# Performance work log

Measured on AMD Instinct MI355X. Metric: run time of the kernel, lower is better.

## Reference

```python
import jax, jax.numpy as jnp
import numpy as np

STATE_LEN = 256
EPS = 1e-5


def _ln(x, g, b):
    m = jnp.mean(x, axis=-1, keepdims=True)
    v = jnp.mean((x - m) ** 2, axis=-1, keepdims=True)
    return (x - m) / jnp.sqrt(v + EPS) * g + b


def setup_inputs() -> dict:
    key = jax.random.key(0)
    ks = jax.random.split(key, 12)
    B, S, L, D, DK, DV = 2, 256, 2048, 512, 64, 64
    T = L + 2 * S  # 2560
    def w(k, i, o):
        return jax.random.normal(k, (i, o), jnp.float32) * 0.02
    return {
        "x": jax.random.normal(ks[0], (B, T, D), jnp.float32),
        "w_q": w(ks[1], D, DK), "w_k": w(ks[2], D, DK), "w_v": w(ks[3], D, DV),
        "w_q_ss": w(ks[4], D, DK), "w_k_ss": w(ks[5], D, DK), "w_v_ss": w(ks[6], D, DV),
        "w_q_se": w(ks[7], D, DK), "w_k_se": w(ks[8], D, DK), "w_v_se": w(ks[9], D, DV),
        "ln_g": jnp.ones((D,), jnp.float32), "ln_b": jnp.zeros((D,), jnp.float32),
        "ln_g_ss": jnp.ones((D,), jnp.float32), "ln_b_ss": jnp.zeros((D,), jnp.float32),
        "ln_g_se": jnp.ones((D,), jnp.float32), "ln_b_se": jnp.zeros((D,), jnp.float32),
        "cope_emb": jax.random.normal(ks[10], (1, DK, T), jnp.float32),
    }


def reference(x, w_q, w_k, w_v, w_q_ss, w_k_ss, w_v_ss, w_q_se, w_k_se, w_v_se,
              ln_g, ln_b, ln_g_ss, ln_b_ss, ln_g_se, ln_b_se, cope_emb):
    S = STATE_LEN
    T = x.shape[1]
    # extract_state: [state_start | main | state_end]
    xs, xm, xe = x[:, :S], x[:, S:T - S], x[:, T - S:]
    xm = _ln(xm, ln_g, ln_b)
    xs = _ln(xs, ln_g_ss, ln_b_ss)
    xe = _ln(xe, ln_g_se, ln_b_se)
    q = jnp.concatenate([xs @ w_q_ss, xm @ w_q, xe @ w_q_se], axis=1)  # [B,T,DK]
    k = jnp.concatenate([xs @ w_k_ss, xm @ w_k, xe @ w_k_se], axis=1)
    v = jnp.concatenate([xs @ w_v_ss, xm @ w_v, xe @ w_v_se], axis=1)
    dk = q.shape[-1]
    # --- CoPE bias ---
    logits = jnp.einsum('btd,bsd->bts', q, k)  # [B,T,T]
    gates = jax.nn.sigmoid(logits)
    # reverse cumsum along keys (flip-cumsum-flip)
    pos = jnp.flip(jnp.cumsum(jnp.flip(gates, -1), axis=-1), -1)
    pos = jnp.minimum(pos, jnp.float32(T - 1))
    pf = jnp.floor(pos)
    pc = jnp.ceil(pos)
    li = jnp.einsum('btd,dm->btm', q, cope_emb[0])  # [B,T,T]
    lc = jnp.take_along_axis(li, pc.astype(jnp.int32), axis=-1)
    lf = jnp.take_along_axis(li, pf.astype(jnp.int32), axis=-1)
    w = pos - pf
    bias = lc * w + lf * (1.0 - w)
    # --- attention with tril-log mask + CoPE bias ---
    causal = jnp.tril(jnp.ones((T, T), dtype=bool))
    att_logits = logits / jnp.sqrt(jnp.float32(dk)) + jnp.where(causal, bias, -jnp.inf)
    attn = jax.nn.softmax(att_logits, axis=-1)
    return jnp.einsum('bts,bsd->btd', attn, v)
```

## Files before the change

### kernel.cpp

```cpp
#include <hip/hip_runtime.h>
#include <hip/hip_bf16.h>
#include <math.h>

using short8 = __attribute__((ext_vector_type(8))) short;
using f32x4  = __attribute__((ext_vector_type(4))) float;

constexpr int S_LEN  = 256;
constexpr int T      = 2560;
constexpr int D_IN   = 512;
constexpr int DK     = 64;
constexpr int B_N    = 2;
constexpr int SS     = 16;

__global__ __launch_bounds__(256) void lnprep_kernel(
    const float* __restrict__ x,
    const float* __restrict__ g_m,  const float* __restrict__ b_m,
    const float* __restrict__ g_s,  const float* __restrict__ b_s,
    const float* __restrict__ g_e,  const float* __restrict__ b_e,
    const float* __restrict__ w_qs, const float* __restrict__ w_ks, const float* __restrict__ w_vs,
    const float* __restrict__ w_q,  const float* __restrict__ w_k,  const float* __restrict__ w_v,
    const float* __restrict__ w_qe, const float* __restrict__ w_ke, const float* __restrict__ w_ve,
    const float* __restrict__ cope,
    __hip_bfloat16* __restrict__ xnh, __hip_bfloat16* __restrict__ xnl,
    __hip_bfloat16* __restrict__ wth, __hip_bfloat16* __restrict__ wtl,
    __hip_bfloat16* __restrict__ copeT)
{
    constexpr int LN_BLOCKS = (B_N * T) / 4;
    if (blockIdx.x < LN_BLOCKS) {
        const int wv   = threadIdx.x >> 6;
        const int lane = threadIdx.x & 63;
        const int row  = blockIdx.x * 4 + wv;
        const int t    = row % T;

        const float *gv, *bv;
        if (t < S_LEN)          { gv = g_s; bv = b_s; }
        else if (t < T - S_LEN) { gv = g_m; bv = b_m; }
        else                    { gv = g_e; bv = b_e; }

        const float4* xr4 = (const float4*)(x + (size_t)row * D_IN);
        float4 a = xr4[lane * 2], b4 = xr4[lane * 2 + 1];
        float xv[8] = {a.x, a.y, a.z, a.w, b4.x, b4.y, b4.z, b4.w};

        float s = 0.f;
#pragma unroll
        for (int j = 0; j < 8; ++j) s += xv[j];
#pragma unroll
        for (int off = 32; off > 0; off >>= 1) s += __shfl_down(s, off);
        s = __shfl(s, 0);
        const float mean = s * (1.0f / D_IN);

        float sq = 0.f;
#pragma unroll
        for (int j = 0; j < 8; ++j) { float d = xv[j] - mean; sq += d * d; }
#pragma unroll
        for (int off = 32; off > 0; off >>= 1) sq += __shfl_down(sq, off);
        sq = __shfl(sq, 0);
        const float inv = rsqrtf(sq * (1.0f / D_IN) + 1e-5f);

        const float4* gv4 = (const float4*)gv;
        const float4* bv4 = (const float4*)bv;
        float4 ga = gv4[lane * 2], gb = gv4[lane * 2 + 1];
        float4 ba = bv4[lane * 2], bb = bv4[lane * 2 + 1];
        float g8[8] = {ga.x, ga.y, ga.z, ga.w, gb.x, gb.y, gb.z, gb.w};
        float b8[8] = {ba.x, ba.y, ba.z, ba.w, bb.x, bb.y, bb.z, bb.w};

        short hs[8], ls[8];
#pragma unroll
        for (int j = 0; j < 8; ++j) {
            float v = (xv[j] - mean) * inv * g8[j] + b8[j];
            __hip_bfloat16 h  = __float2bfloat16(v);
            __hip_bfloat16 lo = __float2bfloat16(v - __bfloat162float(h));
            hs[j] = *(short*)&h;
            ls[j] = *(short*)&lo;
        }
        short8 H = {hs[0],hs[1],hs[2],hs[3],hs[4],hs[5],hs[6],hs[7]};
        short8 L = {ls[0],ls[1],ls[2],ls[3],ls[4],ls[5],ls[6],ls[7]};
        *(short8*)(xnh + (size_t)row * D_IN + lane * 8) = H;
        *(short8*)(xnl + (size_t)row * D_IN + lane * 8) = L;
        return;
    }

    const int i = (blockIdx.x - LN_BLOCKS) * 256 + threadIdx.x;
    constexpr int NW = 9 * DK * D_IN;
    if (i < NW) {
        const int matIdx = i >> 15;
        const int rem = i & 32767;
        const int col = rem >> 9, k = rem & 511;
        const float* W =
            (matIdx == 0) ? w_qs : (matIdx == 1) ? w_ks : (matIdx == 2) ? w_vs :
            (matIdx == 3) ? w_q  : (matIdx == 4) ? w_k  : (matIdx == 5) ? w_v  :
            (matIdx == 6) ? w_qe : (matIdx == 7) ? w_ke : w_ve;
        float f = W[(size_t)k * DK + col];
        __hip_bfloat16 h = __float2bfloat16(f);
        wth[i] = h;
        wtl[i] = __float2bfloat16(f - __bfloat162float(h));
    } else if (i < NW + T * DK) {
        const int j = i - NW;
        const int m = j >> 6, d = j & 63;
        copeT[j] = __float2bfloat16(cope[(size_t)d * T + m]);
    }
}

__global__ __launch_bounds__(256) void qkv_gemm_kernel(
    const __hip_bfloat16* __restrict__ xnh, const __hip_bfloat16* __restrict__ xnl,
    const __hip_bfloat16* __restrict__ wth, const __hip_bfloat16* __restrict__ wtl,
    __hip_bfloat16* __restrict__ qh, __hip_bfloat16* __restrict__ ql,
    __hip_bfloat16* __restrict__ kh, __hip_bfloat16* __restrict__ kl,
    __hip_bfloat16* __restrict__ vT)
{
    const int bid = blockIdx.x;
    const int mt = bid / 3, mat = bid % 3;
    const int r0 = mt * 64;
    const int b  = r0 / T, t0 = r0 % T;
    const int region = (t0 < S_LEN) ? 0 : (t0 < T - S_LEN) ? 1 : 2;
    const int matIdx = region * 3 + mat;

    const int tid = threadIdx.x, lane = tid & 63, wid = tid >> 6;
    const int wm = wid >> 1, wn = wid & 1;
    const int fr = lane & 15, k8 = (lane >> 4) * 8;

    f32x4 acc[2][2];
#pragma unroll
    for (int mf = 0; mf < 2; ++mf)
#pragma unroll
        for (int nf = 0; nf < 2; ++nf) acc[mf][nf] = (f32x4){0.f, 0.f, 0.f, 0.f};

    for (int ks = 0; ks < D_IN / 32; ++ks) {
        const int k = ks * 32 + k8;
        short8 ah[2], al[2], bh2[2], bl2[2];
#pragma unroll
        for (int mf = 0; mf < 2; ++mf) {
            size_t off = (size_t)(r0 + wm * 32 + mf * 16 + fr) * D_IN + k;
            ah[mf] = *(const short8*)(xnh + off);
            al[mf] = *(const short8*)(xnl + off);
        }
#pragma unroll
        for (int nf = 0; nf < 2; ++nf) {
            size_t off = ((size_t)matIdx * DK + wn * 32 + nf * 16 + fr) * D_IN + k;
            bh2[nf] = *(const short8*)(wth + off);
            bl2[nf] = *(const short8*)(wtl + off);
        }
#pragma unroll
        for (int mf = 0; mf < 2; ++mf)
#pragma unroll
            for (int nf = 0; nf < 2; ++nf) {
                acc[mf][nf] = __builtin_amdgcn_mfma_f32_16x16x32_bf16(ah[mf], bh2[nf], acc[mf][nf], 0, 0, 0);
                acc[mf][nf] = __builtin_amdgcn_mfma_f32_16x16x32_bf16(ah[mf], bl2[nf], acc[mf][nf], 0, 0, 0);
                acc[mf][nf] = __builtin_amdgcn_mfma_f32_16x16x32_bf16(al[mf], bh2[nf], acc[mf][nf], 0, 0, 0);
            }
    }

    const int r4 = (lane >> 4) * 4;
#pragma unroll
    for (int mf = 0; mf < 2; ++mf)
#pragma unroll
        for (int nf = 0; nf < 2; ++nf) {
            const int cg = wn * 32 + nf * 16 + fr;
#pragma unroll
            for (int j = 0; j < 4; ++j) {
                const int rg = r0 + wm * 32 + mf * 16 + r4 + j;
                float f = acc[mf][nf][j];
                __hip_bfloat16 h  = __float2bfloat16(f);
                __hip_bfloat16 lo = __float2bfloat16(f - __bfloat162float(h));
                if (mat == 0)      { qh[(size_t)rg * DK + cg] = h; ql[(size_t)rg * DK + cg] = lo; }
                else if (mat == 1) { kh[(size_t)rg * DK + cg] = h; kl[(size_t)rg * DK + cg] = lo; }
                else               { vT[((size_t)b * DK + cg) * T + (rg % T)] = h; }
            }
        }
}

__global__ __launch_bounds__(256) void gemm1_kernel(
    const __hip_bfloat16* __restrict__ qh, const __hip_bfloat16* __restrict__ ql,
    const __hip_bfloat16* __restrict__ kh, const __hip_bfloat16* __restrict__ kl,
    const __hip_bfloat16* __restrict__ copeT,
    float* __restrict__ logc, __hip_bfloat16* __restrict__ lic,
    int b0, int t_off, int TC)
{
    constexpr int TS = T / 64;
    const int per_b = (TC / 128) * TS;
    const int bb  = blockIdx.x / per_b;
    const int rem = blockIdx.x % per_b;
    const int ti  = rem / TS, si = rem % TS;
    const int t0  = ti * 128, s0 = si * 64;
    const int b   = b0 + bb;
    float*          logits_c = logc + (size_t)bb * TC * T;
    __hip_bfloat16* li_c     = lic  + (size_t)bb * TC * T;

    const int tid = threadIdx.x, lane = tid & 63, wid = tid >> 6;
    const int wm  = wid >> 1, wn = wid & 1;
    const int fr  = lane & 15, k8 = (lane >> 4) * 8;
    const size_t qb = (size_t)b * T * DK;

    short8 ah[4][2], al[4][2];
#pragma unroll
    for (int mf = 0; mf < 4; ++mf)
#pragma unroll
        for (int ks = 0; ks < 2; ++ks) {
            size_t off = qb + (size_t)(t_off + t0 + wm * 64 + mf * 16 + fr) * DK + ks * 32 + k8;
            ah[mf][ks] = *(const short8*)(qh + off);
            al[mf][ks] = *(const short8*)(ql + off);
        }
    short8 bh[2][2], bl[2][2], bc[2][2];
#pragma unroll
    for (int nf = 0; nf < 2; ++nf)
#pragma unroll
        for (int ks = 0; ks < 2; ++ks) {
            size_t off = (size_t)(s0 + wn * 32 + nf * 16 + fr) * DK + ks * 32 + k8;
            bh[nf][ks] = *(const short8*)(kh + qb + off);
            bl[nf][ks] = *(const short8*)(kl + qb + off);
            bc[nf][ks] = *(const short8*)(copeT + off);
        }

    f32x4 accL[4][2], accM[4][2];
#pragma unroll
    for (int mf = 0; mf < 4; ++mf)
#pragma unroll
        for (int nf = 0; nf < 2; ++nf) {
            accL[mf][nf] = (f32x4){0.f, 0.f, 0.f, 0.f};
            accM[mf][nf] = (f32x4){0.f, 0.f, 0.f, 0.f};
        }

#pragma unroll
    for (int mf = 0; mf < 4; ++mf)
#pragma unroll
        for (int nf = 0; nf < 2; ++nf)
#pragma unroll
            for (int ks = 0; ks < 2; ++ks) {
                accL[mf][nf] = __builtin_amdgcn_mfma_f32_16x16x32_bf16(ah[mf][ks], bh[nf][ks], accL[mf][nf], 0, 0, 0);
                accL[mf][nf] = __builtin_amdgcn_mfma_f32_16x16x32_bf16(ah[mf][ks], bl[nf][ks], accL[mf][nf], 0, 0, 0);
                accL[mf][nf] = __builtin_amdgcn_mfma_f32_16x16x32_bf16(al[mf][ks], bh[nf][ks], accL[mf][nf], 0, 0, 0);
                accM[mf][nf] = __builtin_amdgcn_mfma_f32_16x16x32_bf16(ah[mf][ks], bc[nf][ks], accM[mf][nf], 0, 0, 0);
            }

    const int r4 = (lane >> 4) * 4;
#pragma unroll
    for (int mf = 0; mf < 4; ++mf)
#pragma unroll
        for (int nf = 0; nf < 2; ++nf) {
            const int cg = s0 + wn * 32 + nf * 16 + fr;
#pragma unroll
            for (int j = 0; j < 4; ++j) {
                const int rl = t0 + wm * 64 + mf * 16 + r4 + j;
                const size_t o = (size_t)rl * T + cg;
                logits_c[o] = accL[mf][nf][j];
                li_c[o]     = __float2bfloat16(accM[mf][nf][j]);
            }
        }
}

__global__ __launch_bounds__(256) void phase2_kernel(
    const float* __restrict__ logc, __hip_bfloat16* __restrict__ lic,
    int t_off, int TC)
{
    constexpr int CH = T / 256;
    const int tid  = threadIdx.x;
    const int lane = tid & 63;
    const int wv   = tid >> 6;
    const int bb   = blockIdx.x / TC;
    const int rl   = blockIdx.x % TC;
    const int t    = t_off + rl;

    __shared__ __hip_bfloat16 sli[T];
    __shared__ float redS[4], redM[4], redE[4];

    const float*    lrow  = logc + ((size_t)bb * TC + rl) * T;
    __hip_bfloat16* lirow = lic  + ((size_t)bb * TC + rl) * T;

#pragma unroll
    for (int i = 0; i < 5; ++i) {
        const int idx = i * 256 + tid;
        ((unsigned int*)sli)[idx] = ((const unsigned int*)lirow)[idx];
    }

    const int s0 = tid * CH;
    float lg[CH], g[CH];
    float lsum = 0.f;
    const float2* lr2 = (const float2*)(lrow + s0);
#pragma unroll
    for (int i = 0; i < 5; ++i) {
        float2 v = lr2[i];
        lg[2 * i] = v.x; lg[2 * i + 1] = v.y;
    }
#pragma unroll
    for (int i = 0; i < CH; ++i) {
        g[i] = 1.0f / (1.0f + __expf(-lg[i]));
        lsum += g[i];
    }

    float incl = lsum;
#pragma unroll
    for (int off = 1; off < 64; off <<= 1) {
        float n = __shfl_up(incl, off);
        if (lane >= off) incl += n;
    }
    if (lane == 63) redS[wv] = incl;
    __syncthreads();
    float total = 0.f, wpre = 0.f;
#pragma unroll
    for (int w2 = 0; w2 < 4; ++w2) {
        float tw = redS[w2];
        total += tw;
        if (w2 < wv) wpre += tw;
    }
    float run = wpre + incl - lsum;

    float att[CH];
    float lmax = -INFINITY;
#pragma unroll
    for (int i = 0; i < CH; ++i) {
        int s = s0 + i;
        float pos = total - run;
        run += g[i];
        pos = fminf(pos, (float)(T - 1));
        float pf = floorf(pos);
        float w  = pos - pf;
        int ipf  = (int)pf;
        int ipc  = (int)ceilf(pos);
        float bias = __bfloat162float(sli[ipc]) * w
                   + __bfloat162float(sli[ipf]) * (1.0f - w);
        float al = lg[i] * 0.125f + bias;
        if (s > t) al = -INFINITY;
        att[i] = al;
        lmax = fmaxf(lmax, al);
    }

#pragma unroll
    for (int off = 32; off > 0; off >>= 1) lmax = fmaxf(lmax, __shfl_down(lmax, off));
    if (lane == 0) redM[wv] = lmax;
    __syncthreads();
    const float bmax = fmaxf(fmaxf(redM[0], redM[1]), fmaxf(redM[2], redM[3]));

    float e[CH];
    float esum = 0.f;
#pragma unroll
    for (int i = 0; i < CH; ++i) {
        e[i] = __expf(att[i] - bmax);
        esum += e[i];
    }
#pragma unroll
    for (int off = 32; off > 0; off >>= 1) esum += __shfl_down(esum, off);
    if (lane == 0) redE[wv] = esum;
    __syncthreads();
    const float rden = 1.0f / (redE[0] + redE[1] + redE[2] + redE[3]);

    unsigned int pw[5];
#pragma unroll
    for (int i = 0; i < 5; ++i) {
        __hip_bfloat16 p0 = __float2bfloat16(e[2 * i] * rden);
        __hip_bfloat16 p1 = __float2bfloat16(e[2 * i + 1] * rden);
        pw[i] = (unsigned int)*(unsigned short*)&p0
              | ((unsigned int)*(unsigned short*)&p1 << 16);
    }
    unsigned int* dst = (unsigned int*)(lirow + s0);
#pragma unroll
    for (int i = 0; i < 5; ++i) dst[i] = pw[i];
}

__global__ __launch_bounds__(256) void gemm2_kernel(
    const __hip_bfloat16* __restrict__ lic, const __hip_bfloat16* __restrict__ vT,
    float* __restrict__ out, int b0, int t_off, int TC)
{
    const int per_b = (TC / 128) * SS;
    const int bb  = blockIdx.x / per_b;
    const int rem = blockIdx.x % per_b;
    const int ti  = rem / SS, sc = rem % SS;
    const int t0  = ti * 128;
    const int sb  = sc * (T / SS);
    if (sb > t_off + t0 + 127) return;
    const int b   = b0 + bb;
    const __hip_bfloat16* p_c = lic + (size_t)bb * TC * T;

    const int tid = threadIdx.x, lane = tid & 63, wid = tid >> 6;
    const int wm  = wid >> 1, wn = wid & 1;
    const int fr  = lane & 15, k8 = (lane >> 4) * 8;
    const size_t vb = (size_t)b * DK * T;

    f32x4 acc[4][2];
#pragma unroll
    for (int mf = 0; mf < 4; ++mf)
#pragma unroll
        for (int nf = 0; nf < 2; ++nf) acc[mf][nf] = (f32x4){0.f, 0.f, 0.f, 0.f};

    for (int ks = 0; ks < (T / SS) / 32; ++ks) {
        const int s = sb + ks * 32 + k8;
        short8 a_p[4], bv[2];
#pragma unroll
        for (int mf = 0; mf < 4; ++mf)
            a_p[mf] = *(const short8*)(p_c + (size_t)(t0 + wm * 64 + mf * 16 + fr) * T + s);
#pragma unroll
        for (int nf = 0; nf < 2; ++nf)
            bv[nf] = *(const short8*)(vT + vb + (size_t)(wn * 32 + nf * 16 + fr) * T + s);
#pragma unroll
        for (int mf = 0; mf < 4; ++mf)
#pragma unroll
            for (int nf = 0; nf < 2; ++nf)
                acc[mf][nf] = __builtin_amdgcn_mfma_f32_16x16x32_bf16(a_p[mf], bv[nf], acc[mf][nf], 0, 0, 0);
    }

    const int r4 = (lane >> 4) * 4;
#pragma unroll
    for (int mf = 0; mf < 4; ++mf)
#pragma unroll
        for (int nf = 0; nf < 2; ++nf) {
            const int cg = wn * 32 + nf * 16 + fr;
#pragma unroll
            for (int j = 0; j < 4; ++j) {
                const int rl = t0 + wm * 64 + mf * 16 + r4 + j;
                atomicAdd(&out[((size_t)b * T + t_off + rl) * DK + cg], acc[mf][nf][j]);
            }
        }
}

extern "C" void kernel_launch(void* const* d_in, const int* in_sizes, int n_in,
                              void* d_out, int out_size, void* d_ws, size_t ws_size,
                              hipStream_t stream)
{
    const float* x    = (const float*)d_in[0];
    const float* w_q  = (const float*)d_in[1];
    const float* w_k  = (const float*)d_in[2];
    const float* w_v  = (const float*)d_in[3];
    const float* w_qs = (const float*)d_in[4];
    const float* w_ks = (const float*)d_in[5];
    const float* w_vs = (const float*)d_in[6];
    const float* w_qe = (const float*)d_in[7];
    const float* w_ke = (const float*)d_in[8];
    const float* w_ve = (const float*)d_in[9];
    const float* g_m  = (const float*)d_in[10];
    const float* b_m  = (const float*)d_in[11];
    const float* g_s  = (const float*)d_in[12];
    const float* b_s  = (const float*)d_in[13];
    const float* g_e  = (const float*)d_in[14];
    const float* b_e  = (const float*)d_in[15];
    const float* cope = (const float*)d_in[16];

    const size_t n_qk  = (size_t)B_N * T * DK;
    const size_t n_xn  = (size_t)B_N * T * D_IN;
    const size_t n_wt  = (size_t)9 * DK * D_IN;
    const size_t fixedB = 5 * n_qk * 2 + (size_t)T * DK * 2
                        + 2 * n_xn * 2 + 2 * n_wt * 2;
    auto chunkB = [&](size_t TC) -> size_t {
        return TC * (size_t)T * 4
             + TC * (size_t)T * 2;
    };
    int TC, NB;
    if (fixedB + 2 * chunkB(T) <= ws_size)       { TC = T;    NB = 2; }
    else if (fixedB + chunkB(T) <= ws_size)      { TC = T;    NB = 1; }
    else if (fixedB + chunkB(1280) <= ws_size)   { TC = 1280; NB = 1; }
    else                                         { TC = 640;  NB = 1; }

    char* w = (char*)d_ws;
    __hip_bfloat16* qh    = (__hip_bfloat16*)w; w += n_qk * 2;
    __hip_bfloat16* ql    = (__hip_bfloat16*)w; w += n_qk * 2;
    __hip_bfloat16* kh    = (__hip_bfloat16*)w; w += n_qk * 2;
    __hip_bfloat16* kl    = (__hip_bfloat16*)w; w += n_qk * 2;
    __hip_bfloat16* vT    = (__hip_bfloat16*)w; w += n_qk * 2;
    __hip_bfloat16* copeT = (__hip_bfloat16*)w; w += (size_t)T * DK * 2;
    __hip_bfloat16* xnh   = (__hip_bfloat16*)w; w += n_xn * 2;
    __hip_bfloat16* xnl   = (__hip_bfloat16*)w; w += n_xn * 2;
    __hip_bfloat16* wth   = (__hip_bfloat16*)w; w += n_wt * 2;
    __hip_bfloat16* wtl   = (__hip_bfloat16*)w; w += n_wt * 2;
    float*          logc  = (float*)w;          w += (size_t)NB * TC * T * 4;
    __hip_bfloat16* lic   = (__hip_bfloat16*)w; w += (size_t)NB * TC * T * 2;

    hipMemsetAsync(d_out, 0, (size_t)out_size * sizeof(float), stream);

    constexpr int LN_BLOCKS   = (B_N * T) / 4;
    const int     PREP_BLOCKS = (int)((n_wt + (size_t)T * DK + 255) / 256);
    lnprep_kernel<<<LN_BLOCKS + PREP_BLOCKS, 256, 0, stream>>>(
        x, g_m, b_m, g_s, b_s, g_e, b_e,
        w_qs, w_ks, w_vs, w_q, w_k, w_v, w_qe, w_ke, w_ve, cope,
        xnh, xnl, wth, wtl, copeT);

    qkv_gemm_kernel<<<(B_N * T / 64) * 3, 256, 0, stream>>>(
        xnh, xnl, wth, wtl, qh, ql, kh, kl, vT);

    for (int b0 = 0; b0 < B_N; b0 += NB)
        for (int t_off = 0; t_off < T; t_off += TC) {
            gemm1_kernel<<<NB * (TC / 128) * (T / 64), 256, 0, stream>>>(
                qh, ql, kh, kl, copeT, logc, lic, b0, t_off, TC);
            phase2_kernel<<<NB * TC, 256, 0, stream>>>(
                logc, lic, t_off, TC);
            gemm2_kernel<<<NB * (TC / 128) * SS, 256, 0, stream>>>(
                lic, vT, (float*)d_out, b0, t_off, TC);
        }
}
```

Measured before the change: 107.2 us.

## Fuse attention stages into one cooperative persistent kernel and fold output zeroing into prep

Merges the gemm1, phase2 and gemm2 launches into a single persistent cooperative kernel that loops over work items and separates the stages with grid-wide barriers, used when the workspace holds both full batches. The output memset is dropped and its zeroing is done by extra blocks in the layer-norm prep kernel. This removes several kernel launches and launch gaps. In exchange, grid.sync costs are added, the grid is capped by occupancy, and a fixed persistent grid may balance the triangular work less well than a full launch.

```diff
diff --git a/kernel.cpp b/kernel.cpp
--- a/kernel.cpp
+++ b/kernel.cpp
@@ -1,6 +1,9 @@
 #include <hip/hip_runtime.h>
+#include <hip/hip_cooperative_groups.h>
 #include <hip/hip_bf16.h>
 #include <math.h>
+
+namespace cg = cooperative_groups;
 
 using short8 = __attribute__((ext_vector_type(8))) short;
 using f32x4  = __attribute__((ext_vector_type(4))) float;
@@ -23,9 +26,12 @@
     const float* __restrict__ cope,
     __hip_bfloat16* __restrict__ xnh, __hip_bfloat16* __restrict__ xnl,
     __hip_bfloat16* __restrict__ wth, __hip_bfloat16* __restrict__ wtl,
-    __hip_bfloat16* __restrict__ copeT)
-{
-    constexpr int LN_BLOCKS = (B_N * T) / 4;
+    __hip_bfloat16* __restrict__ copeT,
+    float* __restrict__ out_zero)
+{
+    constexpr int LN_BLOCKS   = (B_N * T) / 4;
+    constexpr int NW          = 9 * DK * D_IN;
+    constexpr int PREP_BLOCKS = (NW + T * DK + 255) / 256;
     if (blockIdx.x < LN_BLOCKS) {
         const int wv   = threadIdx.x >> 6;
         const int lane = threadIdx.x & 63;
@@ -79,26 +85,30 @@
         *(short8*)(xnl + (size_t)row * D_IN + lane * 8) = L;
         return;
     }
-
-    const int i = (blockIdx.x - LN_BLOCKS) * 256 + threadIdx.x;
-    constexpr int NW = 9 * DK * D_IN;
-    if (i < NW) {
-        const int matIdx = i >> 15;
-        const int rem = i & 32767;
-        const int col = rem >> 9, k = rem & 511;
-        const float* W =
-            (matIdx == 0) ? w_qs : (matIdx == 1) ? w_ks : (matIdx == 2) ? w_vs :
-            (matIdx == 3) ? w_q  : (matIdx == 4) ? w_k  : (matIdx == 5) ? w_v  :
-            (matIdx == 6) ? w_qe : (matIdx == 7) ? w_ke : w_ve;
-        float f = W[(size_t)k * DK + col];
-        __hip_bfloat16 h = __float2bfloat16(f);
-        wth[i] = h;
-        wtl[i] = __float2bfloat16(f - __bfloat162float(h));
-    } else if (i < NW + T * DK) {
-        const int j = i - NW;
-        const int m = j >> 6, d = j & 63;
-        copeT[j] = __float2bfloat16(cope[(size_t)d * T + m]);
-    }
+    if (blockIdx.x < LN_BLOCKS + PREP_BLOCKS) {
+        const int i = (blockIdx.x - LN_BLOCKS) * 256 + threadIdx.x;
+        if (i < NW) {
+            const int matIdx = i >> 15;
+            const int rem = i & 32767;
+            const int col = rem >> 9, k = rem & 511;
+            const float* W =
+                (matIdx == 0) ? w_qs : (matIdx == 1) ? w_ks : (matIdx == 2) ? w_vs :
+                (matIdx == 3) ? w_q  : (matIdx == 4) ? w_k  : (matIdx == 5) ? w_v  :
+                (matIdx == 6) ? w_qe : (matIdx == 7) ? w_ke : w_ve;
+            float f = W[(size_t)k * DK + col];
+            __hip_bfloat16 h = __float2bfloat16(f);
+            wth[i] = h;
+            wtl[i] = __float2bfloat16(f - __bfloat162float(h));
+        } else if (i < NW + T * DK) {
+            const int j = i - NW;
+            const int m = j >> 6, d = j & 63;
+            copeT[j] = __float2bfloat16(cope[(size_t)d * T + m]);
+        }
+        return;
+    }
+    const int z = (blockIdx.x - LN_BLOCKS - PREP_BLOCKS) * 256 + threadIdx.x;
+    if (z < (B_N * T * DK) / 4)
+        ((float4*)out_zero)[z] = make_float4(0.f, 0.f, 0.f, 0.f);
 }
 
 __global__ __launch_bounds__(256) void qkv_gemm_kernel(
@@ -169,23 +179,15 @@
         }
 }
 
-__global__ __launch_bounds__(256) void gemm1_kernel(
+__device__ __forceinline__ void gemm1_body(
+    int bb, int ti, int si,
     const __hip_bfloat16* __restrict__ qh, const __hip_bfloat16* __restrict__ ql,
     const __hip_bfloat16* __restrict__ kh, const __hip_bfloat16* __restrict__ kl,
     const __hip_bfloat16* __restrict__ copeT,
-    float* __restrict__ logc, __hip_bfloat16* __restrict__ lic,
-    int b0, int t_off, int TC)
-{
-    constexpr int TS = T / 64;
-    const int per_b = (TC / 128) * TS;
-    const int bb  = blockIdx.x / per_b;
-    const int rem = blockIdx.x % per_b;
-    const int ti  = rem / TS, si = rem % TS;
+    float* __restrict__ logits_c, __hip_bfloat16* __restrict__ li_c,
+    int b, int t_off)
+{
     const int t0  = ti * 128, s0 = si * 64;
-    const int b   = b0 + bb;
-    float*          logits_c = logc + (size_t)bb * TC * T;
-    __hip_bfloat16* li_c     = lic  + (size_t)bb * TC * T;
-
     const int tid = threadIdx.x, lane = tid & 63, wid = tid >> 6;
     const int wm  = wid >> 1, wn = wid & 1;
     const int fr  = lane & 15, k8 = (lane >> 4) * 8;
@@ -248,23 +250,14 @@
         }
 }
 
-__global__ __launch_bounds__(256) void phase2_kernel(
-    const float* __restrict__ logc, __hip_bfloat16* __restrict__ lic,
-    int t_off, int TC)
+__device__ __forceinline__ void phase2_body(
+    const float* __restrict__ lrow, __hip_bfloat16* __restrict__ lirow, int t,
+    __hip_bfloat16* sli, float* redS, float* redM, float* redE)
 {
     constexpr int CH = T / 256;
     const int tid  = threadIdx.x;
     const int lane = tid & 63;
     const int wv   = tid >> 6;
-    const int bb   = blockIdx.x / TC;
-    const int rl   = blockIdx.x % TC;
-    const int t    = t_off + rl;
-
-    __shared__ __hip_bfloat16 sli[T];
-    __shared__ float redS[4], redM[4], redE[4];
-
-    const float*    lrow  = logc + ((size_t)bb * TC + rl) * T;
-    __hip_bfloat16* lirow = lic  + ((size_t)bb * TC + rl) * T;
 
 #pragma unroll
     for (int i = 0; i < 5; ++i) {
@@ -356,20 +349,14 @@
     for (int i = 0; i < 5; ++i) dst[i] = pw[i];
 }
 
-__global__ __launch_bounds__(256) void gemm2_kernel(
-    const __hip_bfloat16* __restrict__ lic, const __hip_bfloat16* __restrict__ vT,
-    float* __restrict__ out, int b0, int t_off, int TC)
-{
-    const int per_b = (TC / 128) * SS;
-    const int bb  = blockIdx.x / per_b;
-    const int rem = blockIdx.x % per_b;
-    const int ti  = rem / SS, sc = rem % SS;
-    const int t0  = ti * 128;
-    const int sb  = sc * (T / SS);
+__device__ __forceinline__ void gemm2_body(
+    int ti, int sc, const __hip_bfloat16* __restrict__ p_c,
+    const __hip_bfloat16* __restrict__ vT, float* __restrict__ out,
+    int b, int t_off)
+{
+    const int t0 = ti * 128;
+    const int sb = sc * (T / SS);
     if (sb > t_off + t0 + 127) return;
-    const int b   = b0 + bb;
-    const __hip_bfloat16* p_c = lic + (size_t)bb * TC * T;
-
     const int tid = threadIdx.x, lane = tid & 63, wid = tid >> 6;
     const int wm  = wid >> 1, wn = wid & 1;
     const int fr  = lane & 15, k8 = (lane >> 4) * 8;
@@ -409,6 +396,82 @@
                 atomicAdd(&out[((size_t)b * T + t_off + rl) * DK + cg], acc[mf][nf][j]);
             }
         }
+}
+
+__global__ __launch_bounds__(256) void mega_kernel(
+    const __hip_bfloat16* __restrict__ qh, const __hip_bfloat16* __restrict__ ql,
+    const __hip_bfloat16* __restrict__ kh, const __hip_bfloat16* __restrict__ kl,
+    const __hip_bfloat16* __restrict__ copeT, const __hip_bfloat16* __restrict__ vT,
+    float* __restrict__ logc, __hip_bfloat16* __restrict__ lic,
+    float* __restrict__ out)
+{
+    cg::grid_group grid = cg::this_grid();
+    __shared__ __hip_bfloat16 sli[T];
+    __shared__ float redS[4], redM[4], redE[4];
+
+    for (int v = blockIdx.x; v < B_N * (T / 128) * (T / 64); v += gridDim.x) {
+        const int bb  = v / ((T / 128) * (T / 64));
+        const int rem = v % ((T / 128) * (T / 64));
+        gemm1_body(bb, rem / (T / 64), rem % (T / 64),
+                   qh, ql, kh, kl, copeT,
+                   logc + (size_t)bb * T * T, lic + (size_t)bb * T * T, bb, 0);
+    }
+    grid.sync();
+
+    for (int v = blockIdx.x; v < B_N * T; v += gridDim.x) {
+        __syncthreads();
+        const int bb = v / T, rl = v % T;
+        phase2_body(logc + ((size_t)bb * T + rl) * T,
+                    lic  + ((size_t)bb * T + rl) * T, rl,
+                    sli, redS, redM, redE);
+    }
+    grid.sync();
+
+    for (int v = blockIdx.x; v < B_N * (T / 128) * SS; v += gridDim.x) {
+        const int bb  = v / ((T / 128) * SS);
+        const int rem = v % ((T / 128) * SS);
+        gemm2_body(rem / SS, rem % SS, lic + (size_t)bb * T * T, vT, out, bb, 0);
+    }
+}
+
+__global__ __launch_bounds__(256) void gemm1_kernel(
+    const __hip_bfloat16* __restrict__ qh, const __hip_bfloat16* __restrict__ ql,
+    const __hip_bfloat16* __restrict__ kh, const __hip_bfloat16* __restrict__ kl,
+    const __hip_bfloat16* __restrict__ copeT,
+    float* __restrict__ logc, __hip_bfloat16* __restrict__ lic,
+    int b0, int t_off, int TC)
+{
+    constexpr int TS = T / 64;
+    const int per_b = (TC / 128) * TS;
+    const int bb  = blockIdx.x / per_b;
+    const int rem = blockIdx.x % per_b;
+    gemm1_body(bb, rem / TS, rem % TS, qh, ql, kh, kl, copeT,
+               logc + (size_t)bb * TC * T, lic + (size_t)bb * TC * T,
+               b0 + bb, t_off);
+}
+
+__global__ __launch_bounds__(256) void phase2_kernel(
+    const float* __restrict__ logc, __hip_bfloat16* __restrict__ lic,
+    int t_off, int TC)
+{
+    __shared__ __hip_bfloat16 sli[T];
+    __shared__ float redS[4], redM[4], redE[4];
+    const int bb = blockIdx.x / TC;
+    const int rl = blockIdx.x % TC;
+    phase2_body(logc + ((size_t)bb * TC + rl) * T,
+                lic  + ((size_t)bb * TC + rl) * T, t_off + rl,
+                sli, redS, redM, redE);
+}
+
+__global__ __launch_bounds__(256) void gemm2_kernel(
+    const __hip_bfloat16* __restrict__ lic, const __hip_bfloat16* __restrict__ vT,
+    float* __restrict__ out, int b0, int t_off, int TC)
+{
+    const int per_b = (TC / 128) * SS;
+    const int bb  = blockIdx.x / per_b;
+    const int rem = blockIdx.x % per_b;
+    gemm2_body(rem / SS, rem % SS, lic + (size_t)bb * TC * T, vT, out,
+               b0 + bb, t_off);
 }
 
 extern "C" void kernel_launch(void* const* d_in, const int* in_sizes, int n_in,
@@ -432,6 +495,7 @@
     const float* g_e  = (const float*)d_in[14];
     const float* b_e  = (const float*)d_in[15];
     const float* cope = (const float*)d_in[16];
+    float* out = (float*)d_out;
 
     const size_t n_qk  = (size_t)B_N * T * DK;
     const size_t n_xn  = (size_t)B_N * T * D_IN;
@@ -439,8 +503,7 @@
     const size_t fixedB = 5 * n_qk * 2 + (size_t)T * DK * 2
                         + 2 * n_xn * 2 + 2 * n_wt * 2;
     auto chunkB = [&](size_t TC) -> size_t {
-        return TC * (size_t)T * 4
-             + TC * (size_t)T * 2;
+        return TC * (size_t)T * 4 + TC * (size_t)T * 2;
     };
     int TC, NB;
     if (fixedB + 2 * chunkB(T) <= ws_size)       { TC = T;    NB = 2; }
@@ -462,17 +525,36 @@
     float*          logc  = (float*)w;          w += (size_t)NB * TC * T * 4;
     __hip_bfloat16* lic   = (__hip_bfloat16*)w; w += (size_t)NB * TC * T * 2;
 
-    hipMemsetAsync(d_out, 0, (size_t)out_size * sizeof(float), stream);
-
     constexpr int LN_BLOCKS   = (B_N * T) / 4;
-    const int     PREP_BLOCKS = (int)((n_wt + (size_t)T * DK + 255) / 256);
-    lnprep_kernel<<<LN_BLOCKS + PREP_BLOCKS, 256, 0, stream>>>(
+    constexpr int NW          = 9 * DK * D_IN;
+    constexpr int PREP_BLOCKS = (NW + T * DK + 255) / 256;
+    constexpr int ZERO_BLOCKS = ((B_N * T * DK) / 4 + 255) / 256;
+    lnprep_kernel<<<LN_BLOCKS + PREP_BLOCKS + ZERO_BLOCKS, 256, 0, stream>>>(
         x, g_m, b_m, g_s, b_s, g_e, b_e,
         w_qs, w_ks, w_vs, w_q, w_k, w_v, w_qe, w_ke, w_ve, cope,
-        xnh, xnl, wth, wtl, copeT);
+        xnh, xnl, wth, wtl, copeT, out);
 
     qkv_gemm_kernel<<<(B_N * T / 64) * 3, 256, 0, stream>>>(
         xnh, xnl, wth, wtl, qh, ql, kh, kl, vT);
+
+    bool coop = (NB == 2 && TC == T);
+    int maxPerCU = 0;
+    if (coop) {
+        if (hipOccupancyMaxActiveBlocksPerMultiprocessor(
+                &maxPerCU, (const void*)mega_kernel, 256, 0) != hipSuccess
+            || maxPerCU < 1)
+            coop = false;
+    }
+    if (coop) {
+        int grid = maxPerCU * 256;
+        if (grid > 1600) grid = 1600;
+        void* args[] = { (void*)&qh, (void*)&ql, (void*)&kh, (void*)&kl,
+                         (void*)&copeT, (void*)&vT, (void*)&logc, (void*)&lic,
+                         (void*)&out };
+        hipLaunchCooperativeKernel((const void*)mega_kernel,
+                                   dim3(grid), dim3(256), args, 0, stream);
+        return;
+    }
 
     for (int b0 = 0; b0 < B_N; b0 += NB)
         for (int t_off = 0; t_off < T; t_off += TC) {
@@ -481,6 +563,6 @@
             phase2_kernel<<<NB * TC, 256, 0, stream>>>(
                 logc, lic, t_off, TC);
             gemm2_kernel<<<NB * (TC / 128) * SS, 256, 0, stream>>>(
-                lic, vT, (float*)d_out, b0, t_off, TC);
-        }
-}
+                lic, vT, out, b0, t_off, TC);
+        }
+}
```

Result: slower. 217.6 us (+103.0%).
